# Kernel tuning notes

Measured on AMD Instinct MI355X. Metric: run time of the kernel, lower is better.

The kernel has to match this reference:

```python
import jax, jax.numpy as jnp
import numpy as np

D_MODEL = 1024
N_HEADS = 16
D_K = D_MODEL // N_HEADS  # 64
THETA = 10000.0


def _rope(x, token_positions):
    # x: [b, h, s, d], token_positions: [s]
    inv_freq = 1.0 / THETA ** (jnp.arange(0, D_K, 2, dtype=jnp.float32) / D_K)  # [d/2]
    ang = token_positions.astype(jnp.float32)[:, None] * inv_freq               # [s, d/2]
    cos, sin = jnp.cos(ang), jnp.sin(ang)                                       # broadcast over b,h
    x1 = x[..., 0::2]
    x2 = x[..., 1::2]
    even = x1 * cos - x2 * sin
    odd = x1 * sin + x2 * cos
    return jnp.stack([even, odd], axis=-1).reshape(x.shape)  # re-interleave


def setup_inputs() -> dict:
    key = jax.random.key(0)
    k1, k2, k3 = jax.random.split(key, 3)
    B, S = 2, 2048
    x = jax.random.normal(k1, (B, S, D_MODEL), dtype=jnp.float32)
    token_positions = jnp.arange(S, dtype=jnp.int32)
    std_qkv = np.sqrt(2.0 / (D_MODEL + 3 * D_MODEL))
    std_out = np.sqrt(2.0 / (D_MODEL + D_MODEL))
    W_qkv = jax.random.normal(k2, (3 * D_MODEL, D_MODEL), dtype=jnp.float32) * std_qkv
    W_out = jax.random.normal(k3, (D_MODEL, D_MODEL), dtype=jnp.float32) * std_out
    return {"x": x, "token_positions": token_positions, "W_qkv": W_qkv, "W_out": W_out}


def reference(x, token_positions, W_qkv, W_out):
    B, S, _ = x.shape
    qkv = jnp.einsum('bsi,oi->bso', x, W_qkv)                 # [b, s, 3*h*d]
    qkv = qkv.reshape(B, S, 3, N_HEADS, D_K)
    qkv = jnp.transpose(qkv, (2, 0, 3, 1, 4))                 # [3, b, h, s, d]
    q, k, v = qkv[0], qkv[1], qkv[2]
    q = _rope(q, token_positions)
    k = _rope(k, token_positions)
    scores = jnp.einsum('bhqd,bhkd->bhqk', q, k) / jnp.sqrt(jnp.float32(D_K))
    mask = jnp.tril(jnp.ones((S, S), dtype=bool))
    scores = jnp.where(mask, scores, -jnp.inf)
    attn = jax.nn.softmax(scores, axis=-1)
    out = jnp.einsum('bhqk,bhkd->bhqd', attn, v)              # [b, h, s, d]
    out = jnp.transpose(out, (0, 2, 1, 3)).reshape(B, S, D_MODEL)
    return jnp.einsum('bsi,oi->bso', out, W_out)
```

## Files before the change

### kernel.cpp

```cpp
#include <hip/hip_runtime.h>
#include <hip/hip_bf16.h>
#include <math.h>

#define D_MODEL 1024
#define N_HEADS 16
#define D_K     64
#define S_LEN   2048
#define B_SZ    2

typedef unsigned short u16;
typedef unsigned int   u32;
using short8 = __attribute__((ext_vector_type(8))) short;
using f32x4  = __attribute__((ext_vector_type(4))) float;

__device__ inline float bf2f(u16 u) { return __uint_as_float((u32)u << 16); }
__device__ inline u16 f2bf(float f) {
    __hip_bfloat16 h = __float2bfloat16(f);
    return *(u16*)&h;
}
__device__ inline void gload_lds16(const void* g, void* l) {
    __builtin_amdgcn_global_load_lds(
        (const __attribute__((address_space(1))) unsigned int*)g,
        (__attribute__((address_space(3))) unsigned int*)l, 16, 0, 0);
}

__global__ __launch_bounds__(256)
void cast3_f32_bf16(const float* __restrict__ a, u16* __restrict__ ao, int na4,
                    const float* __restrict__ bsrc, u16* __restrict__ bo, int nb4,
                    const float* __restrict__ c, u16* __restrict__ co, int nc4) {
    int j = blockIdx.x * 256 + threadIdx.x;
    const float* src; u16* dst;
    if (j < na4) { src = a; dst = ao; }
    else {
        j -= na4;
        if (j < nb4) { src = bsrc; dst = bo; }
        else {
            j -= nb4;
            if (j >= nc4) return;
            src = c; dst = co;
        }
    }
    float4 v = ((const float4*)src)[j];
    ushort4 u;
    u.x = f2bf(v.x); u.y = f2bf(v.y); u.z = f2bf(v.z); u.w = f2bf(v.w);
    ((ushort4*)dst)[j] = u;
}

template <bool OUT_BF16>
__global__ __launch_bounds__(256)
void gemm_bt_mfma(const u16* __restrict__ A, const u16* __restrict__ B,
                  void* __restrict__ Cout, int M, int N, int K) {
    __shared__ u16 As[128 * 32];
    __shared__ u16 Bs[128 * 32];
    const int tid  = threadIdx.x;
    const int lane = tid & 63;
    const int wv   = tid >> 6;
    const int wm   = wv >> 1, wn = wv & 1;
    const int row0 = blockIdx.y * 128;
    const int col0 = blockIdx.x * 128;

    const int lr = lane >> 2;
    const int lc = (lane & 3) * 8;

    f32x4 acc[4][4] = {};

    for (int k0 = 0; k0 < K; k0 += 32) {
#pragma unroll
        for (int t = 0; t < 2; t++) {
            int rblk = wv * 32 + t * 16;
            gload_lds16(A + (size_t)(row0 + rblk + lr) * K + k0 + lc, &As[rblk * 32]);
            gload_lds16(B + (size_t)(col0 + rblk + lr) * K + k0 + lc, &Bs[rblk * 32]);
        }
        __syncthreads();

        short8 af[4], bfr[4];
#pragma unroll
        for (int mi = 0; mi < 4; mi++)
            af[mi] = *(const short8*)&As[(wm * 64 + mi * 16 + (lane & 15)) * 32 + (lane >> 4) * 8];
#pragma unroll
        for (int nj = 0; nj < 4; nj++)
            bfr[nj] = *(const short8*)&Bs[(wn * 64 + nj * 16 + (lane & 15)) * 32 + (lane >> 4) * 8];
#pragma unroll
        for (int mi = 0; mi < 4; mi++)
#pragma unroll
            for (int nj = 0; nj < 4; nj++)
                acc[mi][nj] = __builtin_amdgcn_mfma_f32_16x16x32_bf16(
                    af[mi], bfr[nj], acc[mi][nj], 0, 0, 0);
        __syncthreads();
    }

    const int cr = (lane >> 4) * 4;
    const int cc = lane & 15;
#pragma unroll
    for (int mi = 0; mi < 4; mi++) {
#pragma unroll
        for (int nj = 0; nj < 4; nj++) {
            int c = col0 + wn * 64 + nj * 16 + cc;
#pragma unroll
            for (int r = 0; r < 4; r++) {
                int rr = row0 + wm * 64 + mi * 16 + cr + r;
                if (OUT_BF16)
                    ((u16*)Cout)[(size_t)rr * N + c] = f2bf(acc[mi][nj][r]);
                else
                    ((float*)Cout)[(size_t)rr * N + c] = acc[mi][nj][r];
            }
        }
    }
}

__global__ __launch_bounds__(256)
void rope_bf16(u16* __restrict__ qkv, const int* __restrict__ pos) {
    int idx = blockIdx.x * blockDim.x + threadIdx.x;
    int j = idx & 31;
    int h = (idx >> 5) & 15;
    int w = (idx >> 9) & 1;
    int s = (idx >> 10) & 2047;
    int b = idx >> 21;

    float p = (float)pos[s];
    float inv_freq = __powf(10000.0f, -(float)(2 * j) / 64.0f);
    float ang = p * inv_freq;
    float sn, cs;
    sincosf(ang, &sn, &cs);
    float sc = (w == 0) ? 0.125f : 1.0f;

    size_t base = (((size_t)(b * S_LEN + s) * 3 + w) * D_MODEL) + h * D_K + 2 * j;
    float x1 = bf2f(qkv[base]);
    float x2 = bf2f(qkv[base + 1]);
    qkv[base]     = f2bf((x1 * cs - x2 * sn) * sc);
    qkv[base + 1] = f2bf((x1 * sn + x2 * cs) * sc);
}

__global__ __launch_bounds__(256)
void vtrans(const u16* __restrict__ qkv, u16* __restrict__ VT) {
    __shared__ u16 t[64][68];
    const int st = blockIdx.x, h = blockIdx.y, b = blockIdx.z;
    const int tid = threadIdx.x;
    const int bh = b * N_HEADS + h;

#pragma unroll
    for (int i = 0; i < 4; i++) {
        int e  = tid + i * 256;
        int sl = e >> 4;
        int c4 = e & 15;
        ushort4 v = *(const ushort4*)&qkv[((size_t)(b * S_LEN + st * 64 + sl) * 3 + 2) * D_MODEL
                                          + h * D_K + c4 * 4];
        *(ushort4*)&t[sl][c4 * 4] = v;
    }
    __syncthreads();
#pragma unroll
    for (int i = 0; i < 4; i++) {
        int e  = tid + i * 256;
        int d  = e >> 4;
        int s4 = e & 15;
        ushort4 o;
        o.x = t[s4 * 4 + 0][d];
        o.y = t[s4 * 4 + 1][d];
        o.z = t[s4 * 4 + 2][d];
        o.w = t[s4 * 4 + 3][d];
        *(ushort4*)&VT[((size_t)bh * D_K + d) * S_LEN + st * 64 + s4 * 4] = o;
    }
}

__device__ __forceinline__ void attn_step(
    const u16* __restrict__ Ksc, const u16* __restrict__ Vsc,
    u16* __restrict__ Psw,
    short8 (&qf)[2], f32x4 (&acc)[4], float& mq, float& lq,
    int k0, int qw0, bool diag, int l15, int quad)
{
    f32x4 s[4] = {};
    __builtin_amdgcn_s_setprio(1);
#pragma unroll
    for (int kf = 0; kf < 2; kf++)
#pragma unroll
        for (int nj = 0; nj < 4; nj++) {
            short8 kfr = *(const short8*)&Ksc[kf * 2048 + (nj * 16 + l15) * 32 + quad * 8];
            s[nj] = __builtin_amdgcn_mfma_f32_16x16x32_bf16(kfr, qf[kf], s[nj], 0, 0, 0);
        }
    __builtin_amdgcn_s_setprio(0);

    if (diag) {
        const int row_g = qw0 + l15;
#pragma unroll
        for (int nj = 0; nj < 4; nj++)
#pragma unroll
            for (int r = 0; r < 4; r++) {
                int key_g = k0 + nj * 16 + quad * 4 + r;
                if (key_g > row_g) s[nj][r] = -INFINITY;
            }
    }

    float rmax = s[0][0];
#pragma unroll
    for (int nj = 0; nj < 4; nj++)
#pragma unroll
        for (int r = 0; r < 4; r++) rmax = fmaxf(rmax, s[nj][r]);
    rmax = fmaxf(rmax, __shfl_xor(rmax, 16, 64));
    rmax = fmaxf(rmax, __shfl_xor(rmax, 32, 64));

    if (!__all(rmax <= mq + 8.f)) {
        float mn = fmaxf(mq, rmax);
        float alpha = __expf(mq - mn);
        mq = mn;
        lq *= alpha;
#pragma unroll
        for (int nj = 0; nj < 4; nj++)
#pragma unroll
            for (int r = 0; r < 4; r++) acc[nj][r] *= alpha;
    }

    float rsum = 0.f;
#pragma unroll
    for (int nj = 0; nj < 4; nj++)
#pragma unroll
        for (int r = 0; r < 4; r++) {
            float p = __expf(s[nj][r] - mq);
            s[nj][r] = p;
            rsum += p;
        }
    rsum += __shfl_xor(rsum, 16, 64);
    rsum += __shfl_xor(rsum, 32, 64);
    lq += rsum;

#pragma unroll
    for (int nj = 0; nj < 4; nj++) {
        u32 lo = ((u32)f2bf(s[nj][1]) << 16) | f2bf(s[nj][0]);
        u32 hi = ((u32)f2bf(s[nj][3]) << 16) | f2bf(s[nj][2]);
        uint2 pk; pk.x = lo; pk.y = hi;
        *(uint2*)&Psw[l15 * 68 + nj * 16 + quad * 4] = pk;
    }

    __builtin_amdgcn_s_setprio(1);
#pragma unroll
    for (int kf = 0; kf < 2; kf++) {
        const u16* pp = &Psw[l15 * 68 + kf * 32 + quad * 8];
        uint2 plo = *(const uint2*)pp;
        uint2 phi = *(const uint2*)(pp + 4);
        u32 praw[4] = { plo.x, plo.y, phi.x, phi.y };
        short8 pf = *(const short8*)praw;
#pragma unroll
        for (int nj = 0; nj < 4; nj++) {
            short8 vf = *(const short8*)&Vsc[kf * 2048 + (nj * 16 + l15) * 32 + quad * 8];
            acc[nj] = __builtin_amdgcn_mfma_f32_16x16x32_bf16(vf, pf, acc[nj], 0, 0, 0);
        }
    }
    __builtin_amdgcn_s_setprio(0);
}

__global__ __launch_bounds__(256)
void attn_mfma(const u16* __restrict__ qkv, const u16* __restrict__ VT,
               u16* __restrict__ out) {
    __shared__ u16 Ks[2][2][64 * 32];
    __shared__ u16 VsT[2][2][64 * 32];
    __shared__ u16 Ps[2][4][16 * 68];

    const int tid  = threadIdx.x;
    const int lane = tid & 63;
    const int wv   = tid >> 6;

    const int bid = blockIdx.x;
    const int idx = bid >> 3;
    const int bh  = (bid & 7) * 4 + (idx >> 4);
    const int pr  = idx & 15;
    const int qtH = 31 - pr;
    const int qtL = pr;
    const int h   = bh & (N_HEADS - 1);
    const int b   = bh >> 4;

    const int l15  = lane & 15;
    const int quad = lane >> 4;
    const int qw0H = qtH * 64 + wv * 16;
    const int qw0L = qtL * 64 + wv * 16;

    const size_t vtb = (size_t)bh * D_K * S_LEN;
    u16* PswH = &Ps[0][wv][0];
    u16* PswL = &Ps[1][wv][0];

    const int lr = lane >> 2;
    const int lc = (lane & 3) * 8;

    short8 qfH[2], qfL[2];
#pragma unroll
    for (int kf = 0; kf < 2; kf++) {
        qfH[kf] = *(const short8*)&qkv[((size_t)(b * S_LEN + qw0H + l15) * 3 + 0) * D_MODEL
                                       + h * D_K + kf * 32 + quad * 8];
        qfL[kf] = *(const short8*)&qkv[((size_t)(b * S_LEN + qw0L + l15) * 3 + 0) * D_MODEL
                                       + h * D_K + kf * 32 + quad * 8];
    }

    f32x4 accH[4] = {}, accL[4] = {};
    float mqH = -INFINITY, lqH = 0.f;
    float mqL = -INFINITY, lqL = 0.f;

    auto STAGE = [&](int kts, int bf) {
        const int k0s = kts * 64;
#pragma unroll
        for (int kf = 0; kf < 2; kf++)
            gload_lds16(qkv + ((size_t)(b * S_LEN + k0s + wv * 16 + lr) * 3 + 1) * D_MODEL
                            + h * D_K + kf * 32 + lc,
                        &Ks[bf][kf][(wv * 16) * 32]);
#pragma unroll
        for (int kc = 0; kc < 2; kc++)
            gload_lds16(VT + vtb + (size_t)(wv * 16 + lr) * S_LEN + k0s + kc * 32 + lc,
                        &VsT[bf][kc][(wv * 16) * 32]);
    };

    STAGE(0, 0);
    __syncthreads();

    int cur = 0;
    for (int kt = 0; kt <= qtH; kt++) {
        const int k0 = kt * 64;

        if (kt < qtH) STAGE(kt + 1, cur ^ 1);

        const u16* Ksc = &Ks[cur][0][0];
        const u16* Vsc = &VsT[cur][0][0];

        attn_step(Ksc, Vsc, PswH, qfH, accH, mqH, lqH,
                  k0, qw0H, kt == qtH, l15, quad);
        if (kt <= qtL)
            attn_step(Ksc, Vsc, PswL, qfL, accL, mqL, lqL,
                      k0, qw0L, kt == qtL, l15, quad);

        __syncthreads();
        cur ^= 1;
    }

    float invlH = 1.f / lqH;
    float invlL = 1.f / lqL;
#pragma unroll
    for (int nj = 0; nj < 4; nj++) {
        ushort4 oH, oL;
        oH.x = f2bf(accH[nj][0] * invlH); oH.y = f2bf(accH[nj][1] * invlH);
        oH.z = f2bf(accH[nj][2] * invlH); oH.w = f2bf(accH[nj][3] * invlH);
        oL.x = f2bf(accL[nj][0] * invlL); oL.y = f2bf(accL[nj][1] * invlL);
        oL.z = f2bf(accL[nj][2] * invlL); oL.w = f2bf(accL[nj][3] * invlL);
        *(ushort4*)&out[(size_t)(b * S_LEN + qw0H + l15) * D_MODEL
                        + h * D_K + nj * 16 + quad * 4] = oH;
        *(ushort4*)&out[(size_t)(b * S_LEN + qw0L + l15) * D_MODEL
                        + h * D_K + nj * 16 + quad * 4] = oL;
    }
}

extern "C" void kernel_launch(void* const* d_in, const int* in_sizes, int n_in,
                              void* d_out, int out_size, void* d_ws, size_t ws_size,
                              hipStream_t stream) {
    const float* x    = (const float*)d_in[0];
    const int*   pos  = (const int*)d_in[1];
    const float* Wqkv = (const float*)d_in[2];
    const float* Wout = (const float*)d_in[3];
    float*       out  = (float*)d_out;

    const int M = B_SZ * S_LEN;

    u16* qkvb = (u16*)d_ws;
    u16* aob  = qkvb + (size_t)M * 3 * D_MODEL;
    u16* xb   = aob  + (size_t)M * D_MODEL;
    u16* wqb  = xb   + (size_t)M * D_MODEL;
    u16* wob  = wqb  + (size_t)3 * D_MODEL * D_MODEL;
    u16* vtb  = wob  + (size_t)D_MODEL * D_MODEL;

    const int na4 = M * D_MODEL / 4;
    const int nb4 = 3 * D_MODEL * D_MODEL / 4;
    const int nc4 = D_MODEL * D_MODEL / 4;
    cast3_f32_bf16<<<(na4 + nb4 + nc4 + 255) / 256, 256, 0, stream>>>(
        x, xb, na4, Wqkv, wqb, nb4, Wout, wob, nc4);

    gemm_bt_mfma<true><<<dim3(3 * D_MODEL / 128, M / 128), 256, 0, stream>>>(
        xb, wqb, qkvb, M, 3 * D_MODEL, D_MODEL);

    rope_bf16<<<(B_SZ * S_LEN * 2 * N_HEADS * 32) / 256, 256, 0, stream>>>(qkvb, pos);

    vtrans<<<dim3(S_LEN / 64, N_HEADS, B_SZ), 256, 0, stream>>>(qkvb, vtb);

    attn_mfma<<<(S_LEN / 64) * N_HEADS * B_SZ / 2, 256, 0, stream>>>(qkvb, vtb, aob);

    gemm_bt_mfma<false><<<dim3(D_MODEL / 128, M / 128), 256, 0, stream>>>(
        aob, wob, out, M, D_MODEL, D_MODEL);
}
```

Before: 221.3 us.

## Split causal attention across two blocks per tile pair with flash-decoding combine

Each pair of query tiles (high and low) is now handled by two blocks instead of one. One block covers key tiles 0-16 of the high query tile. The other covers the remaining key tiles of the high tile and then the whole low tile. Partial outputs and the max/sum statistics for the high tile go to fp32 workspace, and a new combine kernel merges them. This doubles the grid from 512 to 1024 blocks to improve occupancy and load balance on the many CUs. In exchange it adds partial-result traffic and an extra launch, and it drops the K/V double-buffering, so each tile now waits on two barriers with no load/compute overlap.

```diff
diff --git a/kernel.cpp b/kernel.cpp
--- a/kernel.cpp
+++ b/kernel.cpp
@@ -249,97 +249,143 @@
 
 __global__ __launch_bounds__(256)
 void attn_mfma(const u16* __restrict__ qkv, const u16* __restrict__ VT,
-               u16* __restrict__ out) {
-    __shared__ u16 Ks[2][2][64 * 32];
-    __shared__ u16 VsT[2][2][64 * 32];
-    __shared__ u16 Ps[2][4][16 * 68];
+               u16* __restrict__ out, float* __restrict__ partO,
+               float* __restrict__ partML) {
+    __shared__ u16 Ks[2][64 * 32];
+    __shared__ u16 VsT[2][64 * 32];
+    __shared__ u16 Ps[4][16 * 68];
 
     const int tid  = threadIdx.x;
     const int lane = tid & 63;
     const int wv   = tid >> 6;
 
-    const int bid = blockIdx.x;
-    const int idx = bid >> 3;
-    const int bh  = (bid & 7) * 4 + (idx >> 4);
-    const int pr  = idx & 15;
-    const int qtH = 31 - pr;
-    const int qtL = pr;
-    const int h   = bh & (N_HEADS - 1);
-    const int b   = bh >> 4;
+    const int bid  = blockIdx.x;
+    const int idx  = bid >> 3;
+    const int bh   = (bid & 7) * 4 + (idx >> 5);
+    const int rem  = idx & 31;
+    const int pr   = rem >> 1;
+    const int role = rem & 1;
+    const int qtH  = 31 - pr;
+    const int qtL  = pr;
+    const int h    = bh & (N_HEADS - 1);
+    const int b    = bh >> 4;
 
     const int l15  = lane & 15;
     const int quad = lane >> 4;
     const int qw0H = qtH * 64 + wv * 16;
-    const int qw0L = qtL * 64 + wv * 16;
 
     const size_t vtb = (size_t)bh * D_K * S_LEN;
-    u16* PswH = &Ps[0][wv][0];
-    u16* PswL = &Ps[1][wv][0];
-
+    u16* Psw = &Ps[wv][0];
     const int lr = lane >> 2;
     const int lc = (lane & 3) * 8;
 
-    short8 qfH[2], qfL[2];
-#pragma unroll
-    for (int kf = 0; kf < 2; kf++) {
-        qfH[kf] = *(const short8*)&qkv[((size_t)(b * S_LEN + qw0H + l15) * 3 + 0) * D_MODEL
-                                       + h * D_K + kf * 32 + quad * 8];
-        qfL[kf] = *(const short8*)&qkv[((size_t)(b * S_LEN + qw0L + l15) * 3 + 0) * D_MODEL
-                                       + h * D_K + kf * 32 + quad * 8];
-    }
-
-    f32x4 accH[4] = {}, accL[4] = {};
-    float mqH = -INFINITY, lqH = 0.f;
-    float mqL = -INFINITY, lqL = 0.f;
-
-    auto STAGE = [&](int kts, int bf) {
+    auto STAGE = [&](int kts) {
         const int k0s = kts * 64;
 #pragma unroll
         for (int kf = 0; kf < 2; kf++)
             gload_lds16(qkv + ((size_t)(b * S_LEN + k0s + wv * 16 + lr) * 3 + 1) * D_MODEL
                             + h * D_K + kf * 32 + lc,
-                        &Ks[bf][kf][(wv * 16) * 32]);
+                        &Ks[kf][(wv * 16) * 32]);
 #pragma unroll
         for (int kc = 0; kc < 2; kc++)
             gload_lds16(VT + vtb + (size_t)(wv * 16 + lr) * S_LEN + k0s + kc * 32 + lc,
-                        &VsT[bf][kc][(wv * 16) * 32]);
+                        &VsT[kc][(wv * 16) * 32]);
     };
 
-    STAGE(0, 0);
-    __syncthreads();
-
-    int cur = 0;
-    for (int kt = 0; kt <= qtH; kt++) {
-        const int k0 = kt * 64;
-
-        if (kt < qtH) STAGE(kt + 1, cur ^ 1);
-
-        const u16* Ksc = &Ks[cur][0][0];
-        const u16* Vsc = &VsT[cur][0][0];
-
-        attn_step(Ksc, Vsc, PswH, qfH, accH, mqH, lqH,
-                  k0, qw0H, kt == qtH, l15, quad);
-        if (kt <= qtL)
-            attn_step(Ksc, Vsc, PswL, qfL, accL, mqL, lqL,
-                      k0, qw0L, kt == qtL, l15, quad);
-
-        __syncthreads();
-        cur ^= 1;
-    }
-
-    float invlH = 1.f / lqH;
-    float invlL = 1.f / lqL;
+    short8 qfH[2];
+#pragma unroll
+    for (int kf = 0; kf < 2; kf++)
+        qfH[kf] = *(const short8*)&qkv[((size_t)(b * S_LEN + qw0H + l15) * 3 + 0) * D_MODEL
+                                       + h * D_K + kf * 32 + quad * 8];
+    f32x4 accH[4] = {};
+    float mqH = -INFINITY, lqH = 0.f;
+
+    const int kbeg = role ? 17 : 0;
+    const int kend = role ? qtH : 16;
+    for (int kt = kbeg; kt <= kend; kt++) {
+        STAGE(kt);
+        __syncthreads();
+        attn_step(&Ks[0][0], &VsT[0][0], Psw, qfH, accH, mqH, lqH,
+                  kt * 64, qw0H, kt == qtH, l15, quad);
+        __syncthreads();
+    }
+
+    {
+        const size_t unit = (size_t)(bh * 16 + (qtH - 16)) * 2 + role;
+        float* Od = partO + unit * 4096 + (size_t)(wv * 16 + l15) * 64;
+#pragma unroll
+        for (int nj = 0; nj < 4; nj++)
+            *(f32x4*)&Od[nj * 16 + quad * 4] = accH[nj];
+        if (quad == 0) {
+            float* ML = partML + unit * 128;
+            ML[wv * 16 + l15]      = mqH;
+            ML[64 + wv * 16 + l15] = lqH;
+        }
+    }
+
+    if (!role) return;
+
+    const int qw0L = qtL * 64 + wv * 16;
+    short8 qfL[2];
+#pragma unroll
+    for (int kf = 0; kf < 2; kf++)
+        qfL[kf] = *(const short8*)&qkv[((size_t)(b * S_LEN + qw0L + l15) * 3 + 0) * D_MODEL
+                                       + h * D_K + kf * 32 + quad * 8];
+    f32x4 accL[4] = {};
+    float mqL = -INFINITY, lqL = 0.f;
+
+    for (int kt = 0; kt <= qtL; kt++) {
+        STAGE(kt);
+        __syncthreads();
+        attn_step(&Ks[0][0], &VsT[0][0], Psw, qfL, accL, mqL, lqL,
+                  kt * 64, qw0L, kt == qtL, l15, quad);
+        __syncthreads();
+    }
+
+    float invl = 1.f / lqL;
 #pragma unroll
     for (int nj = 0; nj < 4; nj++) {
-        ushort4 oH, oL;
-        oH.x = f2bf(accH[nj][0] * invlH); oH.y = f2bf(accH[nj][1] * invlH);
-        oH.z = f2bf(accH[nj][2] * invlH); oH.w = f2bf(accH[nj][3] * invlH);
-        oL.x = f2bf(accL[nj][0] * invlL); oL.y = f2bf(accL[nj][1] * invlL);
-        oL.z = f2bf(accL[nj][2] * invlL); oL.w = f2bf(accL[nj][3] * invlL);
-        *(ushort4*)&out[(size_t)(b * S_LEN + qw0H + l15) * D_MODEL
-                        + h * D_K + nj * 16 + quad * 4] = oH;
+        ushort4 o;
+        o.x = f2bf(accL[nj][0] * invl); o.y = f2bf(accL[nj][1] * invl);
+        o.z = f2bf(accL[nj][2] * invl); o.w = f2bf(accL[nj][3] * invl);
         *(ushort4*)&out[(size_t)(b * S_LEN + qw0L + l15) * D_MODEL
-                        + h * D_K + nj * 16 + quad * 4] = oL;
+                        + h * D_K + nj * 16 + quad * 4] = o;
+    }
+}
+
+__global__ __launch_bounds__(256)
+void attn_combine(const float* __restrict__ partO, const float* __restrict__ partML,
+                  u16* __restrict__ out) {
+    const int t16 = blockIdx.x & 15;
+    const int bh  = blockIdx.x >> 4;
+    const int h = bh & (N_HEADS - 1), b = bh >> 4;
+    const int q0 = (t16 + 16) * 64;
+    const int tid = threadIdx.x;
+    const int q  = tid >> 2;
+    const int d0 = (tid & 3) * 16;
+
+    const size_t u0 = (size_t)(bh * 16 + t16) * 2;
+    const float* O0 = partO + u0 * 4096;
+    const float* O1 = O0 + 4096;
+    const float* ML0 = partML + u0 * 128;
+    const float* ML1 = ML0 + 128;
+
+    float m0 = ML0[q], l0 = ML0[64 + q];
+    float m1 = ML1[q], l1 = ML1[64 + q];
+    float ms = fmaxf(m0, m1);
+    float f0 = __expf(m0 - ms), f1 = __expf(m1 - ms);
+    float inv = 1.f / (l0 * f0 + l1 * f1);
+    f0 *= inv; f1 *= inv;
+#pragma unroll
+    for (int i = 0; i < 4; i++) {
+        float4 a = *(const float4*)&O0[q * 64 + d0 + i * 4];
+        float4 c = *(const float4*)&O1[q * 64 + d0 + i * 4];
+        ushort4 o;
+        o.x = f2bf(a.x * f0 + c.x * f1);
+        o.y = f2bf(a.y * f0 + c.y * f1);
+        o.z = f2bf(a.z * f0 + c.z * f1);
+        o.w = f2bf(a.w * f0 + c.w * f1);
+        *(ushort4*)&out[(size_t)(b * S_LEN + q0 + q) * D_MODEL + h * D_K + d0 + i * 4] = o;
     }
 }
 
@@ -360,6 +406,8 @@
     u16* wqb  = xb   + (size_t)M * D_MODEL;
     u16* wob  = wqb  + (size_t)3 * D_MODEL * D_MODEL;
     u16* vtb  = wob  + (size_t)D_MODEL * D_MODEL;
+    float* partO  = (float*)(vtb + (size_t)M * D_MODEL);
+    float* partML = partO + (size_t)1024 * 4096;
 
     const int na4 = M * D_MODEL / 4;
     const int nb4 = 3 * D_MODEL * D_MODEL / 4;
@@ -374,7 +422,8 @@
 
     vtrans<<<dim3(S_LEN / 64, N_HEADS, B_SZ), 256, 0, stream>>>(qkvb, vtb);
 
-    attn_mfma<<<(S_LEN / 64) * N_HEADS * B_SZ / 2, 256, 0, stream>>>(qkvb, vtb, aob);
+    attn_mfma<<<1024, 256, 0, stream>>>(qkvb, vtb, aob, partO, partML);
+    attn_combine<<<512, 256, 0, stream>>>(partO, partML, aob);
 
     gemm_bt_mfma<false><<<dim3(D_MODEL / 128, M / 128), 256, 0, stream>>>(
         aob, wob, out, M, D_MODEL, D_MODEL);
```

Result: faster. 216.2 us (-2.3%).
